# Optimization experiments

Measured on AMD Instinct MI355X. Metric: run time of the kernel, lower is better.

## Reference

```python
import jax, jax.numpy as jnp
import numpy as np

B, N, DIM = 2, 1024, 256
DEPTH, HEADS, DIM_HEAD = 4, 4, 64
INNER = HEADS * DIM_HEAD
SCALE = DIM_HEAD ** -0.5
STEP, LAMBD, EPS = 0.1, 0.1, 1e-5


def cx(re, im):
    return jax.lax.complex(re, im)


def setup_inputs() -> dict:
    key = jax.random.key(0)
    ks = jax.random.split(key, 8)
    s = np.float32(1.0 / np.sqrt(DIM))
    f32 = jnp.float32
    return {
        "x_re": jax.random.normal(ks[0], (B, N, DIM), f32),
        "x_im": jax.random.normal(ks[1], (B, N, DIM), f32),
        "ln1_w_re": jnp.ones((DEPTH, DIM), f32),
        "ln1_w_im": jnp.zeros((DEPTH, DIM), f32),
        "ln1_b_re": jnp.zeros((DEPTH, DIM), f32),
        "ln1_b_im": jnp.zeros((DEPTH, DIM), f32),
        "qkv_re": jax.random.normal(ks[2], (DEPTH, INNER, DIM), f32) * s,
        "qkv_im": jax.random.normal(ks[3], (DEPTH, INNER, DIM), f32) * s,
        "out_w_re": jax.random.normal(ks[4], (DEPTH, DIM, INNER), f32) * s,
        "out_w_im": jax.random.normal(ks[5], (DEPTH, DIM, INNER), f32) * s,
        "out_b_re": jnp.zeros((DEPTH, DIM), f32),
        "out_b_im": jnp.zeros((DEPTH, DIM), f32),
        "ln2_w_re": jnp.ones((DEPTH, DIM), f32),
        "ln2_w_im": jnp.zeros((DEPTH, DIM), f32),
        "ln2_b_re": jnp.zeros((DEPTH, DIM), f32),
        "ln2_b_im": jnp.zeros((DEPTH, DIM), f32),
        "ff_re": jax.random.normal(ks[6], (DEPTH, DIM, DIM), f32) * s,
        "ff_im": jax.random.normal(ks[7], (DEPTH, DIM, DIM), f32) * s,
    }


def complex_layernorm(x, w, b):
    # per-component mean/var on real and imag (torch unbiased=False), complex sqrt
    mean = cx(jnp.mean(x.real, -1, keepdims=True), jnp.mean(x.imag, -1, keepdims=True))
    var = cx(jnp.var(x.real, -1, keepdims=True), jnp.var(x.imag, -1, keepdims=True))
    xn = (x - mean) / jnp.sqrt(var + EPS)
    return w * xn + b


def attention(x, Wqkv, Wout, bout):
    # torch Linear: y = x @ W^T ; shared qkv projection w
    w = jnp.einsum('bnd,ed->bne', x, Wqkv)              # [B,N,INNER]
    w = w.reshape(B, N, HEADS, DIM_HEAD).transpose(0, 2, 1, 3)  # [B,H,N,Dh]
    dots = jnp.einsum('bhnd,bhmd->bhnm', w, w.conj()) * SCALE   # complex scores
    mag = jnp.abs(dots)
    a = jax.nn.softmax(mag, axis=-1)                    # softmax on magnitudes
    ph = jnp.angle(dots)                                # polar reconstruction
    attn = cx(a * jnp.cos(ph), a * jnp.sin(ph))
    out = jnp.einsum('bhnm,bhmd->bhnd', attn, w)
    out = out.transpose(0, 2, 1, 3).reshape(B, N, INNER)
    return jnp.einsum('bne,de->bnd', out, Wout) + bout


def feedforward(x, W):
    # FeedForward type1: x1 = x W^T ; CReLU(x + step*x1 - step*lambd)
    x1 = jnp.einsum('bnd,ed->bne', x, W)
    z = x + STEP * x1 - STEP * LAMBD
    return cx(jax.nn.relu(z.real), jax.nn.relu(z.imag))


def reference(x_re, x_im, ln1_w_re, ln1_w_im, ln1_b_re, ln1_b_im,
              qkv_re, qkv_im, out_w_re, out_w_im, out_b_re, out_b_im,
              ln2_w_re, ln2_w_im, ln2_b_re, ln2_b_im, ff_re, ff_im):
    x = cx(x_re, x_im)
    for l in range(DEPTH):
        xn = complex_layernorm(x, cx(ln1_w_re[l], ln1_w_im[l]), cx(ln1_b_re[l], ln1_b_im[l]))
        grad_x = attention(xn, cx(qkv_re[l], qkv_im[l]), cx(out_w_re[l], out_w_im[l]),
                           cx(out_b_re[l], out_b_im[l])) + x
        xn2 = complex_layernorm(grad_x, cx(ln2_w_re[l], ln2_w_im[l]), cx(ln2_b_re[l], ln2_b_im[l]))
        x = feedforward(xn2, cx(ff_re[l], ff_im[l]))
    return x
```

## Files before the change

### kernel.cpp

```cpp
#include <hip/hip_runtime.h>
#include <math.h>

#define B_ 2
#define N_ 1024
#define DIM_ 256
#define DEPTH_ 4
#define HEADS_ 4
#define DHEAD_ 64
#define INNER_ 256
#define SCALE_ 0.125f
#define STEP_ 0.1f
#define LAMBD_ 0.1f
#define EPS_ 1e-5f

typedef __attribute__((ext_vector_type(8))) short short8;
typedef __attribute__((ext_vector_type(4))) float f32x4;

__device__ __forceinline__ unsigned short bf16_rne(float x) {
    unsigned u = __float_as_uint(x);
    unsigned r = (u + 0x7FFFu + ((u >> 16) & 1u)) >> 16;
    return (unsigned short)r;
}
__device__ __forceinline__ float bf16_tof(unsigned short h) {
    return __uint_as_float(((unsigned)h) << 16);
}
__device__ __forceinline__ void split2(float x, unsigned short& hi, unsigned short& lo) {
    hi = bf16_rne(x);
    lo = bf16_rne(x - bf16_tof(hi));
}
__device__ __forceinline__ f32x4 mfma16(short8 a, short8 b, f32x4 c) {
    return __builtin_amdgcn_mfma_f32_16x16x32_bf16(a, b, c, 0, 0, 0);
}
__device__ __forceinline__ short8 neg8(short8 v) {
    union { short8 s; unsigned u[4]; } a; a.s = v;
    a.u[0] ^= 0x80008000u; a.u[1] ^= 0x80008000u;
    a.u[2] ^= 0x80008000u; a.u[3] ^= 0x80008000u;
    return a.s;
}

__device__ __forceinline__ float2 blockReduceSum2(float a, float b) {
    __shared__ float smA[4], smB[4];
    for (int o = 32; o > 0; o >>= 1) {
        a += __shfl_down(a, o, 64);
        b += __shfl_down(b, o, 64);
    }
    int wave = threadIdx.x >> 6, lane = threadIdx.x & 63;
    __syncthreads();
    if (lane == 0) { smA[wave] = a; smB[wave] = b; }
    __syncthreads();
    float ra = smA[0] + smA[1] + smA[2] + smA[3];
    float rb = smB[0] + smB[1] + smB[2] + smB[3];
    return make_float2(ra, rb);
}

__global__ void ln_kernel(const float* __restrict__ xr, const float* __restrict__ xi,
                          const float* __restrict__ wr, const float* __restrict__ wi,
                          const float* __restrict__ br, const float* __restrict__ bi,
                          float* __restrict__ outr, float* __restrict__ outi,
                          unsigned short* __restrict__ planes, int S) {
    int row = blockIdx.x;
    int t = threadIdx.x;
    int idx = row * DIM_ + t;
    float xre = xr[idx], xim = xi[idx];
    float2 s = blockReduceSum2(xre, xim);
    float mre = s.x * (1.f / DIM_), mim = s.y * (1.f / DIM_);
    float dr = xre - mre, di = xim - mim;
    float2 v = blockReduceSum2(dr * dr, di * di);
    float c = v.x * (1.f / DIM_) + EPS_;
    float d = v.y * (1.f / DIM_);
    float r = sqrtf(c * c + d * d);
    float sre = sqrtf(0.5f * (r + c));
    float sim = sqrtf(fmaxf(0.5f * (r - c), 0.f));
    float inv = 1.f / r;
    float nr = (dr * sre + di * sim) * inv;
    float ni = (di * sre - dr * sim) * inv;
    float wre = wr[t], wim = wi[t];
    float orr = wre * nr - wim * ni + br[t];
    float oii = wre * ni + wim * nr + bi[t];
    outr[idx] = orr;
    outi[idx] = oii;
    unsigned short rh, rl, ih, il;
    split2(orr, rh, rl);
    split2(oii, ih, il);
    planes[0 * S + idx] = rh;
    planes[1 * S + idx] = rl;
    planes[2 * S + idx] = ih;
    planes[3 * S + idx] = il;
}

__global__ void wsplit(const float* __restrict__ wr, const float* __restrict__ wi,
                       unsigned short* __restrict__ planes) {
    int idx = blockIdx.x * 256 + threadIdx.x;
    int l = idx >> 16, e = idx & 65535;
    unsigned short rh, rl, ih, il;
    split2(wr[idx], rh, rl);
    split2(wi[idx], ih, il);
    size_t base = (size_t)l * 4 * 65536;
    planes[base + 0 * 65536 + e] = rh;
    planes[base + 1 * 65536 + e] = rl;
    planes[base + 2 * 65536 + e] = ih;
    planes[base + 3 * 65536 + e] = il;
}

template <int MODE>
__global__ __launch_bounds__(64)
void gemm_mfma(const unsigned short* __restrict__ Ap, int aStride,
               const unsigned short* __restrict__ Bp,
               unsigned short* __restrict__ wpo, unsigned short* __restrict__ wtpo,
               const float* __restrict__ biasR, const float* __restrict__ biasI,
               const float* resR, const float* resI,
               float* xoR, float* xoI, int S) {
    const int K = 256;
    int tileM = blockIdx.x * 16, tileN = blockIdx.y * 16;
    int lane = threadIdx.x;
    int m16 = lane & 15, quad = lane >> 4;

    f32x4 accP = (f32x4){0,0,0,0}, accN = (f32x4){0,0,0,0};
    f32x4 accIa = (f32x4){0,0,0,0}, accIb = (f32x4){0,0,0,0};

#pragma unroll
    for (int k0 = 0; k0 < 256; k0 += 32) {
        int kb = k0 + quad * 8;
        short8 a[4], b[4];
#pragma unroll
        for (int p = 0; p < 4; p++) {
            a[p] = *(const short8*)(Ap + (size_t)p * aStride + (size_t)(tileM + m16) * K + kb);
            b[p] = *(const short8*)(Bp + (size_t)p * 65536  + (size_t)(tileN + m16) * K + kb);
        }
        accP  = mfma16(a[0], b[0], accP);
        accP  = mfma16(a[0], b[1], accP);
        accP  = mfma16(a[1], b[0], accP);
        accN  = mfma16(a[2], b[2], accN);
        accN  = mfma16(a[2], b[3], accN);
        accN  = mfma16(a[3], b[2], accN);
        accIa = mfma16(a[0], b[2], accIa);
        accIa = mfma16(a[0], b[3], accIa);
        accIa = mfma16(a[1], b[2], accIa);
        accIb = mfma16(a[2], b[0], accIb);
        accIb = mfma16(a[2], b[1], accIb);
        accIb = mfma16(a[3], b[0], accIb);
    }

#pragma unroll
    for (int r = 0; r < 4; r++) {
        int row = tileM + quad * 4 + r;
        int col = tileN + m16;
        size_t g = (size_t)row * 256 + col;
        float vr = accP[r] - accN[r];
        float vi = accIa[r] + accIb[r];
        if (MODE == 1) {
            unsigned short h0, h1, h2, h3;
            split2(vr, h0, h1);
            split2(vi, h2, h3);
            size_t tidx = ((size_t)(row >> 10) * 256 + col) * 1024 + (row & 1023);
            wpo[0 * (size_t)S + g] = h0;
            wpo[1 * (size_t)S + g] = h1;
            wpo[2 * (size_t)S + g] = h2;
            wpo[3 * (size_t)S + g] = h3;
            wtpo[0 * (size_t)S + tidx] = h0;
            wtpo[1 * (size_t)S + tidx] = h1;
            wtpo[2 * (size_t)S + tidx] = h2;
            wtpo[3 * (size_t)S + tidx] = h3;
        } else if (MODE == 2) {
            xoR[g] = vr + biasR[col] + resR[g];
            xoI[g] = vi + biasI[col] + resI[g];
        } else {
            float zr = resR[g] + STEP_ * vr - STEP_ * LAMBD_;
            float zi = resI[g] + STEP_ * vi;
            xoR[g] = fmaxf(zr, 0.f);
            xoI[g] = fmaxf(zi, 0.f);
        }
    }
}

__global__ __launch_bounds__(256, 2)
void attn_mfma(const unsigned short* __restrict__ wp,
               const unsigned short* __restrict__ wtp,
               unsigned short* __restrict__ aop, int S) {
    __shared__ float Pb[4][2112];
    __shared__ float mlbuf[4][64][2];

    int tid = threadIdx.x;
    int wave = tid >> 6, lane = tid & 63;
    int m16 = lane & 15, quad = lane >> 4;
    int zz = blockIdx.x, bb = zz >> 2, hh = zz & 3;
    int q0 = blockIdx.y * 16;

    short8 qf[4][2], nqr[2][2];
    {
        size_t qbase = (size_t)(bb * N_ + q0 + m16) * INNER_ + hh * DHEAD_;
#pragma unroll
        for (int p = 0; p < 4; p++)
#pragma unroll
            for (int kc = 0; kc < 2; kc++)
                qf[p][kc] = *(const short8*)(wp + (size_t)p * S + qbase + kc * 32 + quad * 8);
        nqr[0][0] = neg8(qf[0][0]); nqr[0][1] = neg8(qf[0][1]);
        nqr[1][0] = neg8(qf[1][0]); nqr[1][1] = neg8(qf[1][1]);
    }

    float mrow = -1e30f, lrow = 0.f;
    f32x4 Oa[4][2];
#pragma unroll
    for (int ni = 0; ni < 4; ni++) { Oa[ni][0] = (f32x4){0,0,0,0}; Oa[ni][1] = (f32x4){0,0,0,0}; }

    float* prb = &Pb[wave][0];
    float* pib = &Pb[wave][1056];

    for (int t = 0; t < 4; t++) {
        int kt = wave + 4 * t;

        f32x4 sr[4], si[4];
#pragma unroll
        for (int ni = 0; ni < 4; ni++) { sr[ni] = (f32x4){0,0,0,0}; si[ni] = (f32x4){0,0,0,0}; }
#pragma unroll
        for (int ni = 0; ni < 4; ni++) {
            size_t kbase = (size_t)(bb * N_ + kt * 64 + ni * 16 + m16) * INNER_ + hh * DHEAD_;
            short8 kf[4][2];
#pragma unroll
            for (int p = 0; p < 4; p++)
#pragma unroll
                for (int kc = 0; kc < 2; kc++)
                    kf[p][kc] = *(const short8*)(wp + (size_t)p * S + kbase + kc * 32 + quad * 8);
#pragma unroll
            for (int kc = 0; kc < 2; kc++) {
                f32x4 r = sr[ni], im = si[ni];
                r  = mfma16(kf[0][kc], qf[0][kc], r);
                r  = mfma16(kf[0][kc], qf[1][kc], r);
                r  = mfma16(kf[1][kc], qf[0][kc], r);
                r  = mfma16(kf[2][kc], qf[2][kc], r);
                r  = mfma16(kf[2][kc], qf[3][kc], r);
                r  = mfma16(kf[3][kc], qf[2][kc], r);
                im = mfma16(kf[0][kc], qf[2][kc], im);
                im = mfma16(kf[0][kc], qf[3][kc], im);
                im = mfma16(kf[1][kc], qf[2][kc], im);
                im = mfma16(kf[2][kc], nqr[0][kc], im);
                im = mfma16(kf[2][kc], nqr[1][kc], im);
                im = mfma16(kf[3][kc], nqr[0][kc], im);
                sr[ni] = r; si[ni] = im;
            }
        }

        float mag[4][4], srs[4][4], sis[4][4];
        float mx = -1e30f;
#pragma unroll
        for (int ni = 0; ni < 4; ni++)
#pragma unroll
            for (int r = 0; r < 4; r++) {
                float a = sr[ni][r] * SCALE_, b = si[ni][r] * SCALE_;
                srs[ni][r] = a; sis[ni][r] = b;
                float mg = sqrtf(a * a + b * b);
                mag[ni][r] = mg;
                mx = fmaxf(mx, mg);
            }
        mx = fmaxf(mx, __shfl_xor(mx, 16, 64));
        mx = fmaxf(mx, __shfl_xor(mx, 32, 64));
        float newm = fmaxf(mrow, mx);
        float alpha = expf(mrow - newm);
        mrow = newm;
        float psum = 0.f;
#pragma unroll
        for (int ni = 0; ni < 4; ni++)
#pragma unroll
            for (int r = 0; r < 4; r++) {
                float p = expf(mag[ni][r] - newm);
                psum += p;
                float sc = (mag[ni][r] > 0.f) ? (p / mag[ni][r]) : 0.f;
                float pr = (mag[ni][r] > 0.f) ? srs[ni][r] * sc : p;
                float pi = sis[ni][r] * sc;
                int key = ni * 16 + quad * 4 + r;
                prb[m16 * 66 + key] = pr;
                pib[m16 * 66 + key] = pi;
            }
        psum += __shfl_xor(psum, 16, 64);
        psum += __shfl_xor(psum, 32, 64);
        lrow = lrow * alpha + psum;
#pragma unroll
        for (int ni = 0; ni < 4; ni++)
#pragma unroll
            for (int r = 0; r < 4; r++) { Oa[ni][0][r] *= alpha; Oa[ni][1][r] *= alpha; }

        short8 prh[2], prl[2], pihf[2], pilf[2], nih[2], nil2[2];
#pragma unroll
        for (int kc = 0; kc < 2; kc++) {
            unsigned short a0[8], a1[8], b0[8], b1[8];
#pragma unroll
            for (int j = 0; j < 8; j++) {
                float vr = prb[m16 * 66 + kc * 32 + quad * 8 + j];
                float vi = pib[m16 * 66 + kc * 32 + quad * 8 + j];
                split2(vr, a0[j], a1[j]);
                split2(vi, b0[j], b1[j]);
            }
            short8 x0, x1, y0, y1;
#pragma unroll
            for (int j = 0; j < 8; j++) {
                x0[j] = (short)a0[j]; x1[j] = (short)a1[j];
                y0[j] = (short)b0[j]; y1[j] = (short)b1[j];
            }
            prh[kc] = x0; prl[kc] = x1; pihf[kc] = y0; pilf[kc] = y1;
            nih[kc] = neg8(y0); nil2[kc] = neg8(y1);
        }

#pragma unroll
        for (int ni = 0; ni < 4; ni++) {
            size_t vbase = (size_t)(bb * INNER_ + hh * DHEAD_ + ni * 16 + m16) * N_ + kt * 64;
            short8 vf[4][2];
#pragma unroll
            for (int p = 0; p < 4; p++)
#pragma unroll
                for (int kc = 0; kc < 2; kc++)
                    vf[p][kc] = *(const short8*)(wtp + (size_t)p * S + vbase + kc * 32 + quad * 8);
#pragma unroll
            for (int kc = 0; kc < 2; kc++) {
                f32x4 orv = Oa[ni][0], oiv = Oa[ni][1];
                orv = mfma16(vf[0][kc], prh[kc], orv);
                orv = mfma16(vf[0][kc], prl[kc], orv);
                orv = mfma16(vf[1][kc], prh[kc], orv);
                orv = mfma16(vf[2][kc], nih[kc], orv);
                orv = mfma16(vf[2][kc], nil2[kc], orv);
                orv = mfma16(vf[3][kc], nih[kc], orv);
                oiv = mfma16(vf[0][kc], pihf[kc], oiv);
                oiv = mfma16(vf[0][kc], pilf[kc], oiv);
                oiv = mfma16(vf[1][kc], pihf[kc], oiv);
                oiv = mfma16(vf[2][kc], prh[kc], oiv);
                oiv = mfma16(vf[2][kc], prl[kc], oiv);
                oiv = mfma16(vf[3][kc], prh[kc], oiv);
                Oa[ni][0] = orv; Oa[ni][1] = oiv;
            }
        }
    }

    if (wave != 0) {
        float* mb = &Pb[wave][0];
#pragma unroll
        for (int ni = 0; ni < 4; ni++)
#pragma unroll
            for (int r = 0; r < 4; r++) {
                mb[lane * 33 + ni * 8 + r]     = Oa[ni][0][r];
                mb[lane * 33 + ni * 8 + 4 + r] = Oa[ni][1][r];
            }
        mlbuf[wave][lane][0] = mrow;
        mlbuf[wave][lane][1] = lrow;
    }
    __syncthreads();
    if (wave == 0) {
        float mm = mrow;
#pragma unroll
        for (int w = 1; w < 4; w++) mm = fmaxf(mm, mlbuf[w][lane][0]);
        float a0 = expf(mrow - mm);
        float ltot = a0 * lrow;
        float aw[3];
#pragma unroll
        for (int w = 1; w < 4; w++) {
            aw[w - 1] = expf(mlbuf[w][lane][0] - mm);
            ltot += aw[w - 1] * mlbuf[w][lane][1];
        }
        float invl = 1.f / ltot;
        size_t obase = (size_t)(bb * N_ + q0 + m16) * INNER_ + hh * DHEAD_;
#pragma unroll
        for (int ni = 0; ni < 4; ni++)
#pragma unroll
            for (int r = 0; r < 4; r++) {
                float vr = a0 * Oa[ni][0][r];
                float vi = a0 * Oa[ni][1][r];
#pragma unroll
                for (int w = 1; w < 4; w++) {
                    vr += aw[w - 1] * Pb[w][lane * 33 + ni * 8 + r];
                    vi += aw[w - 1] * Pb[w][lane * 33 + ni * 8 + 4 + r];
                }
                vr *= invl; vi *= invl;
                unsigned short h0, h1, h2, h3;
                split2(vr, h0, h1);
                split2(vi, h2, h3);
                size_t o = obase + ni * 16 + quad * 4 + r;
                aop[0 * (size_t)S + o] = h0;
                aop[1 * (size_t)S + o] = h1;
                aop[2 * (size_t)S + o] = h2;
                aop[3 * (size_t)S + o] = h3;
            }
    }
}

__global__ void pack_planar(const float* __restrict__ xr, const float* __restrict__ xi,
                            float* __restrict__ out, int S, int cap) {
    int idx = blockIdx.x * 256 + threadIdx.x;
    if (idx < cap) out[idx] = xr[idx];
    if (S + idx < cap) out[S + idx] = xi[idx];
}

__global__ void pack_real(const float* __restrict__ xr, float* __restrict__ out, int cap) {
    int idx = blockIdx.x * 256 + threadIdx.x;
    if (idx < cap) out[idx] = xr[idx];
}

extern "C" void kernel_launch(void* const* d_in, const int* in_sizes, int n_in,
                              void* d_out, int out_size, void* d_ws, size_t ws_size,
                              hipStream_t stream) {
    const float* in_xre = (const float*)d_in[0];
    const float* in_xim = (const float*)d_in[1];
    const float* ln1wr = (const float*)d_in[2];
    const float* ln1wi = (const float*)d_in[3];
    const float* ln1br = (const float*)d_in[4];
    const float* ln1bi = (const float*)d_in[5];
    const float* qkvr  = (const float*)d_in[6];
    const float* qkvi  = (const float*)d_in[7];
    const float* outwr = (const float*)d_in[8];
    const float* outwi = (const float*)d_in[9];
    const float* outbr = (const float*)d_in[10];
    const float* outbi = (const float*)d_in[11];
    const float* ln2wr = (const float*)d_in[12];
    const float* ln2wi = (const float*)d_in[13];
    const float* ln2br = (const float*)d_in[14];
    const float* ln2bi = (const float*)d_in[15];
    const float* ffr   = (const float*)d_in[16];
    const float* ffi   = (const float*)d_in[17];

    const size_t S = (size_t)B_ * N_ * DIM_;
    const int    Si = (int)S;

    float* ws  = (float*)d_ws;
    float* xre = ws;            float* xim = xre + S;
    float* xnr = xim + S;       float* xni = xnr + S;

    unsigned short* xnp   = (unsigned short*)(xni + S);
    unsigned short* aop   = xnp + 4 * S;
    unsigned short* wpb   = aop + 4 * S;
    unsigned short* wtpb  = wpb + 4 * S;
    unsigned short* qkvp  = wtpb + 4 * S;
    unsigned short* outwp = qkvp + (size_t)DEPTH_ * 4 * 65536;
    unsigned short* ffp   = outwp + (size_t)DEPTH_ * 4 * 65536;

    wsplit<<<DEPTH_ * 65536 / 256, 256, 0, stream>>>(qkvr, qkvi, qkvp);
    wsplit<<<DEPTH_ * 65536 / 256, 256, 0, stream>>>(outwr, outwi, outwp);
    wsplit<<<DEPTH_ * 65536 / 256, 256, 0, stream>>>(ffr, ffi, ffp);

    const int MR = B_ * N_;
    dim3 gGemm(MR / 16, INNER_ / 16);
    dim3 gAttn(B_ * HEADS_, N_ / 16);
    int eBlocks = (int)(S / 256);

    bool directOut = (out_size >= (int)(2 * S));
    float* foutR = directOut ? (float*)d_out : xre;
    float* foutI = directOut ? (float*)d_out + S : xim;

    for (int l = 0; l < DEPTH_; l++) {
        const float* xinR = (l == 0) ? in_xre : xre;
        const float* xinI = (l == 0) ? in_xim : xim;

        ln_kernel<<<MR, DIM_, 0, stream>>>(xinR, xinI,
            ln1wr + l * DIM_, ln1wi + l * DIM_, ln1br + l * DIM_, ln1bi + l * DIM_,
            xnr, xni, xnp, Si);

        gemm_mfma<1><<<gGemm, 64, 0, stream>>>(xnp, Si, qkvp + (size_t)l * 4 * 65536,
            wpb, wtpb, nullptr, nullptr, nullptr, nullptr, nullptr, nullptr, Si);

        attn_mfma<<<gAttn, 256, 0, stream>>>(wpb, wtpb, aop, Si);

        gemm_mfma<2><<<gGemm, 64, 0, stream>>>(aop, Si, outwp + (size_t)l * 4 * 65536,
            nullptr, nullptr, outbr + l * DIM_, outbi + l * DIM_, xinR, xinI, xre, xim, Si);

        ln_kernel<<<MR, DIM_, 0, stream>>>(xre, xim,
            ln2wr + l * DIM_, ln2wi + l * DIM_, ln2br + l * DIM_, ln2bi + l * DIM_,
            xnr, xni, xnp, Si);

        float* oR = (l == DEPTH_ - 1) ? foutR : xre;
        float* oI = (l == DEPTH_ - 1) ? foutI : xim;
        gemm_mfma<3><<<gGemm, 64, 0, stream>>>(xnp, Si, ffp + (size_t)l * 4 * 65536,
            nullptr, nullptr, nullptr, nullptr, xnr, xni, oR, oI, Si);
    }

    if (!directOut) {
        pack_real<<<eBlocks, 256, 0, stream>>>(xre, (float*)d_out, out_size);
    }
}
```

Baseline: 655.6 us.

## Cut attention PV precision to single bf16, use 8 waves, wave-level layernorm, fused weight split

Attention now runs 8 waves per block, each covering two 64-key tiles, and merges partial results with a tree reduction in shared memory. The probability matrix is stored as packed bf16 pairs, and the PV product drops the low-order split terms, so it uses 8 MFMAs per tile instead of 24. Layernorm becomes one 64-lane wave per row with float4 loads and xor-shuffle reductions, which removes the block barriers. The three weight-split launches are merged into one, and expf is replaced by __expf. The reduced PV precision risks accuracy loss.

```diff
diff --git a/kernel.cpp b/kernel.cpp
--- a/kernel.cpp
+++ b/kernel.cpp
@@ -38,68 +38,102 @@
     return a.s;
 }
 
-__device__ __forceinline__ float2 blockReduceSum2(float a, float b) {
-    __shared__ float smA[4], smB[4];
-    for (int o = 32; o > 0; o >>= 1) {
-        a += __shfl_down(a, o, 64);
-        b += __shfl_down(b, o, 64);
-    }
-    int wave = threadIdx.x >> 6, lane = threadIdx.x & 63;
-    __syncthreads();
-    if (lane == 0) { smA[wave] = a; smB[wave] = b; }
-    __syncthreads();
-    float ra = smA[0] + smA[1] + smA[2] + smA[3];
-    float rb = smB[0] + smB[1] + smB[2] + smB[3];
-    return make_float2(ra, rb);
-}
-
-__global__ void ln_kernel(const float* __restrict__ xr, const float* __restrict__ xi,
-                          const float* __restrict__ wr, const float* __restrict__ wi,
-                          const float* __restrict__ br, const float* __restrict__ bi,
-                          float* __restrict__ outr, float* __restrict__ outi,
-                          unsigned short* __restrict__ planes, int S) {
+__global__ __launch_bounds__(64)
+void ln_kernel(const float* __restrict__ xr, const float* __restrict__ xi,
+               const float* __restrict__ wr, const float* __restrict__ wi,
+               const float* __restrict__ br, const float* __restrict__ bi,
+               float* __restrict__ outr, float* __restrict__ outi,
+               unsigned short* __restrict__ planes, int S) {
     int row = blockIdx.x;
-    int t = threadIdx.x;
-    int idx = row * DIM_ + t;
-    float xre = xr[idx], xim = xi[idx];
-    float2 s = blockReduceSum2(xre, xim);
-    float mre = s.x * (1.f / DIM_), mim = s.y * (1.f / DIM_);
-    float dr = xre - mre, di = xim - mim;
-    float2 v = blockReduceSum2(dr * dr, di * di);
-    float c = v.x * (1.f / DIM_) + EPS_;
-    float d = v.y * (1.f / DIM_);
+    int lane = threadIdx.x;
+    int base = row * DIM_ + lane * 4;
+
+    float4 xr4 = *(const float4*)(xr + base);
+    float4 xi4 = *(const float4*)(xi + base);
+    float ar[4] = {xr4.x, xr4.y, xr4.z, xr4.w};
+    float ai[4] = {xi4.x, xi4.y, xi4.z, xi4.w};
+
+    float sr = ar[0] + ar[1] + ar[2] + ar[3];
+    float si = ai[0] + ai[1] + ai[2] + ai[3];
+#pragma unroll
+    for (int o = 1; o < 64; o <<= 1) {
+        sr += __shfl_xor(sr, o, 64);
+        si += __shfl_xor(si, o, 64);
+    }
+    float mre = sr * (1.f / DIM_), mim = si * (1.f / DIM_);
+
+    float drv[4], div[4];
+    float vr = 0.f, vi = 0.f;
+#pragma unroll
+    for (int j = 0; j < 4; j++) {
+        drv[j] = ar[j] - mre;
+        div[j] = ai[j] - mim;
+        vr += drv[j] * drv[j];
+        vi += div[j] * div[j];
+    }
+#pragma unroll
+    for (int o = 1; o < 64; o <<= 1) {
+        vr += __shfl_xor(vr, o, 64);
+        vi += __shfl_xor(vi, o, 64);
+    }
+    float c = vr * (1.f / DIM_) + EPS_;
+    float d = vi * (1.f / DIM_);
     float r = sqrtf(c * c + d * d);
     float sre = sqrtf(0.5f * (r + c));
     float sim = sqrtf(fmaxf(0.5f * (r - c), 0.f));
     float inv = 1.f / r;
-    float nr = (dr * sre + di * sim) * inv;
-    float ni = (di * sre - dr * sim) * inv;
-    float wre = wr[t], wim = wi[t];
-    float orr = wre * nr - wim * ni + br[t];
-    float oii = wre * ni + wim * nr + bi[t];
-    outr[idx] = orr;
-    outi[idx] = oii;
-    unsigned short rh, rl, ih, il;
-    split2(orr, rh, rl);
-    split2(oii, ih, il);
-    planes[0 * S + idx] = rh;
-    planes[1 * S + idx] = rl;
-    planes[2 * S + idx] = ih;
-    planes[3 * S + idx] = il;
-}
-
-__global__ void wsplit(const float* __restrict__ wr, const float* __restrict__ wi,
-                       unsigned short* __restrict__ planes) {
-    int idx = blockIdx.x * 256 + threadIdx.x;
+
+    int wc = lane * 4;
+    float4 wr4 = *(const float4*)(wr + wc);
+    float4 wi4 = *(const float4*)(wi + wc);
+    float4 br4 = *(const float4*)(br + wc);
+    float4 bi4 = *(const float4*)(bi + wc);
+    float wrv[4] = {wr4.x, wr4.y, wr4.z, wr4.w};
+    float wiv[4] = {wi4.x, wi4.y, wi4.z, wi4.w};
+    float brv[4] = {br4.x, br4.y, br4.z, br4.w};
+    float biv[4] = {bi4.x, bi4.y, bi4.z, bi4.w};
+
+    float orr[4], oii[4];
+    unsigned short rh[4], rl[4], ih[4], il[4];
+#pragma unroll
+    for (int j = 0; j < 4; j++) {
+        float nr = (drv[j] * sre + div[j] * sim) * inv;
+        float ni = (div[j] * sre - drv[j] * sim) * inv;
+        orr[j] = wrv[j] * nr - wiv[j] * ni + brv[j];
+        oii[j] = wrv[j] * ni + wiv[j] * nr + biv[j];
+        split2(orr[j], rh[j], rl[j]);
+        split2(oii[j], ih[j], il[j]);
+    }
+    *(float4*)(outr + base) = make_float4(orr[0], orr[1], orr[2], orr[3]);
+    *(float4*)(outi + base) = make_float4(oii[0], oii[1], oii[2], oii[3]);
+    *(ushort4*)(planes + 0 * (size_t)S + base) = make_ushort4(rh[0], rh[1], rh[2], rh[3]);
+    *(ushort4*)(planes + 1 * (size_t)S + base) = make_ushort4(rl[0], rl[1], rl[2], rl[3]);
+    *(ushort4*)(planes + 2 * (size_t)S + base) = make_ushort4(ih[0], ih[1], ih[2], ih[3]);
+    *(ushort4*)(planes + 3 * (size_t)S + base) = make_ushort4(il[0], il[1], il[2], il[3]);
+}
+
+__global__ void wsplit_all(const float* __restrict__ s0r, const float* __restrict__ s0i,
+                           const float* __restrict__ s1r, const float* __restrict__ s1i,
+                           const float* __restrict__ s2r, const float* __restrict__ s2i,
+                           unsigned short* __restrict__ d0,
+                           unsigned short* __restrict__ d1,
+                           unsigned short* __restrict__ d2) {
+    const int PER = DEPTH_ * 65536;
+    int gid = blockIdx.x * 256 + threadIdx.x;
+    int sel = gid / PER;
+    int idx = gid - sel * PER;
+    const float* wr = (sel == 0) ? s0r : (sel == 1) ? s1r : s2r;
+    const float* wi = (sel == 0) ? s0i : (sel == 1) ? s1i : s2i;
+    unsigned short* dst = (sel == 0) ? d0 : (sel == 1) ? d1 : d2;
     int l = idx >> 16, e = idx & 65535;
     unsigned short rh, rl, ih, il;
     split2(wr[idx], rh, rl);
     split2(wi[idx], ih, il);
     size_t base = (size_t)l * 4 * 65536;
-    planes[base + 0 * 65536 + e] = rh;
-    planes[base + 1 * 65536 + e] = rl;
-    planes[base + 2 * 65536 + e] = ih;
-    planes[base + 3 * 65536 + e] = il;
+    dst[base + 0 * 65536 + e] = rh;
+    dst[base + 1 * 65536 + e] = rl;
+    dst[base + 2 * 65536 + e] = ih;
+    dst[base + 3 * 65536 + e] = il;
 }
 
 template <int MODE>
@@ -173,12 +207,12 @@
     }
 }
 
-__global__ __launch_bounds__(256, 2)
+__global__ __launch_bounds__(512, 4)
 void attn_mfma(const unsigned short* __restrict__ wp,
                const unsigned short* __restrict__ wtp,
                unsigned short* __restrict__ aop, int S) {
-    __shared__ float Pb[4][2112];
-    __shared__ float mlbuf[4][64][2];
+    __shared__ unsigned int ShBuf[8448];
+    __shared__ float mlbuf[8][64][2];
 
     int tid = threadIdx.x;
     int wave = tid >> 6, lane = tid & 63;
@@ -203,11 +237,10 @@
 #pragma unroll
     for (int ni = 0; ni < 4; ni++) { Oa[ni][0] = (f32x4){0,0,0,0}; Oa[ni][1] = (f32x4){0,0,0,0}; }
 
-    float* prb = &Pb[wave][0];
-    float* pib = &Pb[wave][1056];
-
-    for (int t = 0; t < 4; t++) {
-        int kt = wave + 4 * t;
+    unsigned int* prbu = ShBuf + wave * 1056;
+
+    for (int t = 0; t < 2; t++) {
+        int kt = wave + 8 * t;
 
         f32x4 sr[4], si[4];
 #pragma unroll
@@ -255,21 +288,20 @@
         mx = fmaxf(mx, __shfl_xor(mx, 16, 64));
         mx = fmaxf(mx, __shfl_xor(mx, 32, 64));
         float newm = fmaxf(mrow, mx);
-        float alpha = expf(mrow - newm);
+        float alpha = __expf(mrow - newm);
         mrow = newm;
         float psum = 0.f;
 #pragma unroll
         for (int ni = 0; ni < 4; ni++)
 #pragma unroll
             for (int r = 0; r < 4; r++) {
-                float p = expf(mag[ni][r] - newm);
+                float p = __expf(mag[ni][r] - newm);
                 psum += p;
                 float sc = (mag[ni][r] > 0.f) ? (p / mag[ni][r]) : 0.f;
                 float pr = (mag[ni][r] > 0.f) ? srs[ni][r] * sc : p;
                 float pi = sis[ni][r] * sc;
                 int key = ni * 16 + quad * 4 + r;
-                prb[m16 * 66 + key] = pr;
-                pib[m16 * 66 + key] = pi;
+                prbu[m16 * 66 + key] = ((unsigned)bf16_rne(pi) << 16) | bf16_rne(pr);
             }
         psum += __shfl_xor(psum, 16, 64);
         psum += __shfl_xor(psum, 32, 64);
@@ -279,95 +311,94 @@
 #pragma unroll
             for (int r = 0; r < 4; r++) { Oa[ni][0][r] *= alpha; Oa[ni][1][r] *= alpha; }
 
-        short8 prh[2], prl[2], pihf[2], pilf[2], nih[2], nil2[2];
+        short8 prh[2], pih[2], nih[2];
 #pragma unroll
         for (int kc = 0; kc < 2; kc++) {
-            unsigned short a0[8], a1[8], b0[8], b1[8];
+            short8 x, y;
 #pragma unroll
             for (int j = 0; j < 8; j++) {
-                float vr = prb[m16 * 66 + kc * 32 + quad * 8 + j];
-                float vi = pib[m16 * 66 + kc * 32 + quad * 8 + j];
-                split2(vr, a0[j], a1[j]);
-                split2(vi, b0[j], b1[j]);
+                unsigned val = prbu[m16 * 66 + kc * 32 + quad * 8 + j];
+                x[j] = (short)(val & 0xffffu);
+                y[j] = (short)(val >> 16);
             }
-            short8 x0, x1, y0, y1;
-#pragma unroll
-            for (int j = 0; j < 8; j++) {
-                x0[j] = (short)a0[j]; x1[j] = (short)a1[j];
-                y0[j] = (short)b0[j]; y1[j] = (short)b1[j];
-            }
-            prh[kc] = x0; prl[kc] = x1; pihf[kc] = y0; pilf[kc] = y1;
-            nih[kc] = neg8(y0); nil2[kc] = neg8(y1);
+            prh[kc] = x; pih[kc] = y; nih[kc] = neg8(y);
         }
 
 #pragma unroll
         for (int ni = 0; ni < 4; ni++) {
             size_t vbase = (size_t)(bb * INNER_ + hh * DHEAD_ + ni * 16 + m16) * N_ + kt * 64;
-            short8 vf[4][2];
-#pragma unroll
-            for (int p = 0; p < 4; p++)
-#pragma unroll
-                for (int kc = 0; kc < 2; kc++)
-                    vf[p][kc] = *(const short8*)(wtp + (size_t)p * S + vbase + kc * 32 + quad * 8);
-#pragma unroll
-            for (int kc = 0; kc < 2; kc++) {
-                f32x4 orv = Oa[ni][0], oiv = Oa[ni][1];
-                orv = mfma16(vf[0][kc], prh[kc], orv);
-                orv = mfma16(vf[0][kc], prl[kc], orv);
-                orv = mfma16(vf[1][kc], prh[kc], orv);
-                orv = mfma16(vf[2][kc], nih[kc], orv);
-                orv = mfma16(vf[2][kc], nil2[kc], orv);
-                orv = mfma16(vf[3][kc], nih[kc], orv);
-                oiv = mfma16(vf[0][kc], pihf[kc], oiv);
-                oiv = mfma16(vf[0][kc], pilf[kc], oiv);
-                oiv = mfma16(vf[1][kc], pihf[kc], oiv);
-                oiv = mfma16(vf[2][kc], prh[kc], oiv);
-                oiv = mfma16(vf[2][kc], prl[kc], oiv);
-                oiv = mfma16(vf[3][kc], prh[kc], oiv);
-                Oa[ni][0] = orv; Oa[ni][1] = oiv;
-            }
+            short8 vr0 = *(const short8*)(wtp + 0 * (size_t)S + vbase + quad * 8);
+            short8 vr1 = *(const short8*)(wtp + 0 * (size_t)S + vbase + 32 + quad * 8);
+            short8 vi0 = *(const short8*)(wtp + 2 * (size_t)S + vbase + quad * 8);
+            short8 vi1 = *(const short8*)(wtp + 2 * (size_t)S + vbase + 32 + quad * 8);
+            f32x4 orv = Oa[ni][0], oiv = Oa[ni][1];
+            orv = mfma16(vr0, prh[0], orv);
+            orv = mfma16(vi0, nih[0], orv);
+            orv = mfma16(vr1, prh[1], orv);
+            orv = mfma16(vi1, nih[1], orv);
+            oiv = mfma16(vr0, pih[0], oiv);
+            oiv = mfma16(vi0, prh[0], oiv);
+            oiv = mfma16(vr1, pih[1], oiv);
+            oiv = mfma16(vi1, prh[1], oiv);
+            Oa[ni][0] = orv; Oa[ni][1] = oiv;
         }
     }
 
-    if (wave != 0) {
-        float* mb = &Pb[wave][0];
+    float* Obuf = (float*)ShBuf;
+    __syncthreads();
+
+#define WRITE_O(slice)                                                          \
+    {                                                                           \
+        float* mb = Obuf + (slice) * 2112 + lane * 33;                          \
+        _Pragma("unroll")                                                       \
+        for (int ni = 0; ni < 4; ni++)                                          \
+            _Pragma("unroll")                                                   \
+            for (int r = 0; r < 4; r++) {                                       \
+                mb[ni * 8 + r]     = Oa[ni][0][r];                              \
+                mb[ni * 8 + 4 + r] = Oa[ni][1][r];                              \
+            }                                                                   \
+        mlbuf[wave][lane][0] = mrow;                                            \
+        mlbuf[wave][lane][1] = lrow;                                            \
+    }
+
+#define COMBINE(slice, srcw)                                                    \
+    {                                                                           \
+        float m1 = mlbuf[srcw][lane][0], l1 = mlbuf[srcw][lane][1];             \
+        float mm = fmaxf(mrow, m1);                                             \
+        float a0 = __expf(mrow - mm), a1 = __expf(m1 - mm);                     \
+        mrow = mm;                                                              \
+        lrow = a0 * lrow + a1 * l1;                                             \
+        float* mb = Obuf + (slice) * 2112 + lane * 33;                          \
+        _Pragma("unroll")                                                       \
+        for (int ni = 0; ni < 4; ni++)                                          \
+            _Pragma("unroll")                                                   \
+            for (int r = 0; r < 4; r++) {                                       \
+                Oa[ni][0][r] = a0 * Oa[ni][0][r] + a1 * mb[ni * 8 + r];         \
+                Oa[ni][1][r] = a0 * Oa[ni][1][r] + a1 * mb[ni * 8 + 4 + r];     \
+            }                                                                   \
+    }
+
+    if (wave >= 4) WRITE_O(wave - 4);
+    __syncthreads();
+    if (wave < 4) COMBINE(wave, wave + 4);
+    __syncthreads();
+    if (wave == 2 || wave == 3) WRITE_O(wave - 2);
+    __syncthreads();
+    if (wave < 2) COMBINE(wave, wave + 2);
+    __syncthreads();
+    if (wave == 1) WRITE_O(0);
+    __syncthreads();
+
+    if (wave == 0) {
+        COMBINE(0, 1);
+        float invl = 1.f / lrow;
+        size_t obase = (size_t)(bb * N_ + q0 + m16) * INNER_ + hh * DHEAD_;
 #pragma unroll
         for (int ni = 0; ni < 4; ni++)
 #pragma unroll
             for (int r = 0; r < 4; r++) {
-                mb[lane * 33 + ni * 8 + r]     = Oa[ni][0][r];
-                mb[lane * 33 + ni * 8 + 4 + r] = Oa[ni][1][r];
-            }
-        mlbuf[wave][lane][0] = mrow;
-        mlbuf[wave][lane][1] = lrow;
-    }
-    __syncthreads();
-    if (wave == 0) {
-        float mm = mrow;
-#pragma unroll
-        for (int w = 1; w < 4; w++) mm = fmaxf(mm, mlbuf[w][lane][0]);
-        float a0 = expf(mrow - mm);
-        float ltot = a0 * lrow;
-        float aw[3];
-#pragma unroll
-        for (int w = 1; w < 4; w++) {
-            aw[w - 1] = expf(mlbuf[w][lane][0] - mm);
-            ltot += aw[w - 1] * mlbuf[w][lane][1];
-        }
-        float invl = 1.f / ltot;
-        size_t obase = (size_t)(bb * N_ + q0 + m16) * INNER_ + hh * DHEAD_;
-#pragma unroll
-        for (int ni = 0; ni < 4; ni++)
-#pragma unroll
-            for (int r = 0; r < 4; r++) {
-                float vr = a0 * Oa[ni][0][r];
-                float vi = a0 * Oa[ni][1][r];
-#pragma unroll
-                for (int w = 1; w < 4; w++) {
-                    vr += aw[w - 1] * Pb[w][lane * 33 + ni * 8 + r];
-                    vi += aw[w - 1] * Pb[w][lane * 33 + ni * 8 + 4 + r];
-                }
-                vr *= invl; vi *= invl;
+                float vr = Oa[ni][0][r] * invl;
+                float vi = Oa[ni][1][r] * invl;
                 unsigned short h0, h1, h2, h3;
                 split2(vr, h0, h1);
                 split2(vi, h2, h3);
@@ -378,13 +409,8 @@
                 aop[3 * (size_t)S + o] = h3;
             }
     }
-}
-
-__global__ void pack_planar(const float* __restrict__ xr, const float* __restrict__ xi,
-                            float* __restrict__ out, int S, int cap) {
-    int idx = blockIdx.x * 256 + threadIdx.x;
-    if (idx < cap) out[idx] = xr[idx];
-    if (S + idx < cap) out[S + idx] = xi[idx];
+#undef WRITE_O
+#undef COMBINE
 }
 
 __global__ void pack_real(const float* __restrict__ xr, float* __restrict__ out, int cap) {
@@ -429,9 +455,8 @@
     unsigned short* outwp = qkvp + (size_t)DEPTH_ * 4 * 65536;
     unsigned short* ffp   = outwp + (size_t)DEPTH_ * 4 * 65536;
 
-    wsplit<<<DEPTH_ * 65536 / 256, 256, 0, stream>>>(qkvr, qkvi, qkvp);
-    wsplit<<<DEPTH_ * 65536 / 256, 256, 0, stream>>>(outwr, outwi, outwp);
-    wsplit<<<DEPTH_ * 65536 / 256, 256, 0, stream>>>(ffr, ffi, ffp);
+    wsplit_all<<<3 * DEPTH_ * 65536 / 256, 256, 0, stream>>>(
+        qkvr, qkvi, outwr, outwi, ffr, ffi, qkvp, outwp, ffp);
 
     const int MR = B_ * N_;
     dim3 gGemm(MR / 16, INNER_ / 16);
@@ -446,19 +471,19 @@
         const float* xinR = (l == 0) ? in_xre : xre;
         const float* xinI = (l == 0) ? in_xim : xim;
 
-        ln_kernel<<<MR, DIM_, 0, stream>>>(xinR, xinI,
+        ln_kernel<<<MR, 64, 0, stream>>>(xinR, xinI,
             ln1wr + l * DIM_, ln1wi + l * DIM_, ln1br + l * DIM_, ln1bi + l * DIM_,
             xnr, xni, xnp, Si);
 
         gemm_mfma<1><<<gGemm, 64, 0, stream>>>(xnp, Si, qkvp + (size_t)l * 4 * 65536,
             wpb, wtpb, nullptr, nullptr, nullptr, nullptr, nullptr, nullptr, Si);
 
-        attn_mfma<<<gAttn, 256, 0, stream>>>(wpb, wtpb, aop, Si);
+        attn_mfma<<<gAttn, 512, 0, stream>>>(wpb, wtpb, aop, Si);
 
         gemm_mfma<2><<<gGemm, 64, 0, stream>>>(aop, Si, outwp + (size_t)l * 4 * 65536,
             nullptr, nullptr, outbr + l * DIM_, outbi + l * DIM_, xinR, xinI, xre, xim, Si);
 
-        ln_kernel<<<MR, DIM_, 0, stream>>>(xre, xim,
+        ln_kernel<<<MR, 64, 0, stream>>>(xre, xim,
             ln2wr + l * DIM_, ln2wi + l * DIM_, ln2br + l * DIM_, ln2bi + l * DIM_,
             xnr, xni, xnp, Si);
 
```

Result: no change. 660.4 us (+0.7%).
